# Optimization experiments

Hardware: AMD Instinct MI355X
Metric: run time of the kernel (lower is better)

The kernel has to match this reference:

```python
import jax, jax.numpy as jnp
import numpy as np

EPS = 1e-5

def _conv3x3(x, w, b):
    # NCHW, OIHW, 3x3 stride 1 pad 1
    y = jax.lax.conv_general_dilated(x, w, window_strides=(1, 1),
                                     padding=((1, 1), (1, 1)),
                                     dimension_numbers=('NCHW', 'OIHW', 'NCHW'))
    return y + b[None, :, None, None]

def _pool_upsample(x, k):
    # adaptive avg pool to (H/k, W/k) then nearest block-upsample back
    B, C, H, W = x.shape
    p = x.reshape(B, C, H // k, k, W // k, k).mean(axis=(3, 5))
    return jnp.repeat(jnp.repeat(p, k, axis=2), k, axis=3)

def setup_inputs() -> dict:
    key = jax.random.key(0)
    ks = jax.random.split(key, 12)
    B, C, H, W = 32, 8, 300, 300
    d = {
        'x': jax.random.normal(ks[0], (B, C, H, W), jnp.float32),
        'w5': jax.random.normal(ks[1], (8, 16, 3, 3), jnp.float32) * 0.1,
        'b5': jnp.zeros((8,), jnp.float32),
        'w10': jax.random.normal(ks[2], (8, 16, 3, 3), jnp.float32) * 0.1,
        'b10': jnp.zeros((8,), jnp.float32),
        'w15': jax.random.normal(ks[3], (8, 16, 3, 3), jnp.float32) * 0.1,
        'b15': jnp.zeros((8,), jnp.float32),
        'gw': jax.random.normal(ks[4], (8, 24, 3, 3), jnp.float32) * 0.1,
        'gb': jnp.zeros((8,), jnp.float32),
        'mw': jax.random.normal(ks[5], (8, 24, 3, 3), jnp.float32) * 0.1,
        'mb': jnp.zeros((8,), jnp.float32),
        'gamma': jnp.ones((8,), jnp.float32),
        'beta': jnp.zeros((8,), jnp.float32),
    }
    return d

def reference(x, w5, b5, w10, b10, w15, b15, gw, gb, mw, mb, gamma, beta):
    up5 = _pool_upsample(x, 5)    # [B,8,300,300]
    up10 = _pool_upsample(x, 10)
    up15 = _pool_upsample(x, 15)
    c5 = _conv3x3(jnp.concatenate([x, up5], axis=1), w5, b5)
    c10 = _conv3x3(jnp.concatenate([x, up10], axis=1), w10, b10)
    c15 = _conv3x3(jnp.concatenate([x, up15], axis=1), w15, b15)
    g_in = jnp.concatenate([c5, c10, c15], axis=1)  # [B,24,H,W]
    # gated conv, activation=None: conv(g_in) * sigmoid(mask_conv(g_in))
    y = _conv3x3(g_in, gw, gb) * jax.nn.sigmoid(_conv3x3(g_in, mw, mb))
    # batch norm (training-mode batch stats, biased var, as torch default)
    mean = y.mean(axis=(0, 2, 3), keepdims=True)
    var = ((y - mean) ** 2).mean(axis=(0, 2, 3), keepdims=True)
    y = (y - mean) * jax.lax.rsqrt(var + EPS)
    return y * gamma[None, :, None, None] + beta[None, :, None, None]
```

## Files before the change

kernel.cpp:

```cpp
#include <hip/hip_runtime.h>
#include <math.h>

typedef __bf16 bfrag __attribute__((ext_vector_type(8)));
typedef __bf16 bf16x4 __attribute__((ext_vector_type(4)));
typedef __bf16 bf16x8 __attribute__((ext_vector_type(8)));
typedef float f32x4 __attribute__((ext_vector_type(4)));

#define BN 32
#define HH 300
#define WW 300
#define HW 90000
#define NPX (BN * HW)

#define GX 10
#define GY 19

#define P5I_BYTE_OFF   0
#define P10I_BYTE_OFF  1843200
#define P15I_BYTE_OFF  2304000
#define CWB_BYTE_OFF   2508800
#define GWB_BYTE_OFF   2524160
#define STAT_BYTE_OFF  2531328
#define SS_BYTE_OFF    2539520
#define XBF_BYTE_OFF   2539584
#define XBF_END        (XBF_BYTE_OFF + (size_t)NPX * 16)

__device__ __forceinline__ short f2bf(float f) {
    union { float f; unsigned u; } v;
    v.f = f;
    unsigned r = v.u + 0x7FFF + ((v.u >> 16) & 1);
    return (short)(r >> 16);
}

__device__ __forceinline__ float bf2f(unsigned short s) {
    union { unsigned u; float f; } v;
    v.u = ((unsigned)s) << 16;
    return v.f;
}

__global__ void k_setup(const float* __restrict__ w5, const float* __restrict__ w10,
                        const float* __restrict__ w15, const float* __restrict__ gw,
                        const float* __restrict__ mw, short* __restrict__ cBg,
                        short* __restrict__ gBg, double* __restrict__ stats) {
    int t = threadIdx.x;
    for (int idx = t; idx < 7680; idx += 256) {
        int s = idx / 2560, rem = idx % 2560;
        int n = rem / 160, r2 = rem % 160;
        int tap = r2 / 16, ci = r2 % 16;
        float v = 0.f;
        if (n < 8 && tap < 9) {
            const float* W = (s == 0) ? w5 : ((s == 1) ? w10 : w15);
            v = W[(n * 16 + ci) * 9 + tap];
        }
        cBg[idx] = f2bf(v);
    }
    for (int idx = t; idx < 3584; idx += 256) {
        int n = idx / 224, r2 = idx % 224;
        int blk = r2 / 8, cj = r2 % 8;
        float v = 0.f;
        if (blk < 27) {
            int tap = blk / 3, ci24 = (blk % 3) * 8 + cj;
            if (n < 8) v = gw[(n * 24 + ci24) * 9 + tap];
            else       v = mw[((n - 8) * 24 + ci24) * 9 + tap];
        }
        gBg[idx] = f2bf(v);
    }
    for (int idx = t; idx < 16 * 64; idx += 256) stats[idx] = 0.0;
}

__global__ void k_pool5(const float* __restrict__ x, unsigned short* __restrict__ p5i) {
    int id = blockIdx.x * 256 + threadIdx.x;
    int bc = id / 3600, cell = id % 3600;
    int b = bc >> 3, c = bc & 7;
    int pi = cell / 60, pj = cell % 60;
    const float* rp = x + (size_t)bc * HW + pi * 5 * WW + pj * 5;
    float s = 0.f;
#pragma unroll
    for (int u = 0; u < 5; u++)
#pragma unroll
        for (int v = 0; v < 5; v++) s += rp[u * WW + v];
    p5i[((size_t)b * 3600 + cell) * 8 + c] = (unsigned short)f2bf(s * 0.04f);
}

__global__ __launch_bounds__(256) void k_prep(const float* __restrict__ x,
                                              unsigned short* __restrict__ xbf,
                                              unsigned short* __restrict__ p5i) {
    __shared__ float tf[8][5][304];
    const int t = threadIdx.x;
    const int pi = blockIdx.x, b = blockIdx.y;
    for (int idx = t; idx < 3000; idx += 256) {
        int ch = idx / 375, rem = idx % 375;
        int r = rem / 75, j = rem % 75;
        float4 v = *(const float4*)&x[((size_t)(b * 8 + ch) * HH + pi * 5 + r) * WW + 4 * j];
        *(float4*)&tf[ch][r][4 * j] = v;
    }
    __syncthreads();
    for (int idx = t; idx < 1500; idx += 256) {
        int r = idx / 300, c = idx - r * 300;
        bf16x8 pk;
#pragma unroll
        for (int ch = 0; ch < 8; ch++) pk[ch] = (__bf16)tf[ch][r][c];
        *(bf16x8*)&xbf[((size_t)b * HW + (pi * 5 + r) * WW + c) * 8] = pk;
    }
    for (int idx = t; idx < 512; idx += 256) {
        int ch = idx >> 6, pj = idx & 63;
        if (pj < 60) {
            float s = 0.f;
#pragma unroll
            for (int u = 0; u < 5; u++)
#pragma unroll
                for (int v = 0; v < 5; v++) s += tf[ch][u][pj * 5 + v];
            p5i[((size_t)b * 3600 + pi * 60 + pj) * 8 + ch] = (unsigned short)f2bf(s * 0.04f);
        }
    }
}

__global__ void k_poolD(const unsigned short* __restrict__ p5i,
                        unsigned short* __restrict__ p10i,
                        unsigned short* __restrict__ p15i) {
    int id = blockIdx.x * 256 + threadIdx.x;
    if (id < 230400) {
        int bc = id / 900, cell = id % 900;
        int b = bc >> 3, c = bc & 7;
        int pi = cell / 30, pj = cell % 30;
        const unsigned short* base = p5i + ((size_t)b * 3600) * 8 + c;
        float s = bf2f(base[((2 * pi) * 60 + 2 * pj) * 8]) +
                  bf2f(base[((2 * pi) * 60 + 2 * pj + 1) * 8]) +
                  bf2f(base[((2 * pi + 1) * 60 + 2 * pj) * 8]) +
                  bf2f(base[((2 * pi + 1) * 60 + 2 * pj + 1) * 8]);
        p10i[((size_t)b * 900 + cell) * 8 + c] = (unsigned short)f2bf(s * 0.25f);
    } else if (id < 332800) {
        int id2 = id - 230400;
        int bc = id2 / 400, cell = id2 % 400;
        int b = bc >> 3, c = bc & 7;
        int pi = cell / 20, pj = cell % 20;
        const unsigned short* base = p5i + ((size_t)b * 3600) * 8 + c;
        float s = 0.f;
#pragma unroll
        for (int u = 0; u < 3; u++)
#pragma unroll
            for (int v = 0; v < 3; v++)
                s += bf2f(base[((3 * pi + u) * 60 + 3 * pj + v) * 8]);
        p15i[((size_t)b * 400 + cell) * 8 + c] = (unsigned short)f2bf(s * (1.f / 9.f));
    }
}

template <int K, int PW>
__device__ __forceinline__ void up_load(const unsigned short* __restrict__ pooled,
                                        int b, int r0, int c0, int t, uint4* v) {
#pragma unroll
    for (int it = 0; it < 3; it++) {
        int idx = t + 256 * it;
        uint4 val = {0u, 0u, 0u, 0u};
        if (idx < 720) {
            int i = idx / 36, j = idx - i * 36;
            int ra = r0 - 2 + i, ca = c0 - 2 + j;
            if (ra >= 0 && ra < HH && ca >= 0 && ca < WW) {
                int pi = (int)((unsigned)ra / K);
                int pj = (int)((unsigned)ca / K);
                val = *(const uint4*)&pooled[((size_t)b * (PW * PW) + pi * PW + pj) * 8];
            }
        }
        v[it] = val;
    }
}

__device__ __forceinline__ void up_store(short* xuU, int t, const uint4* v) {
#pragma unroll
    for (int it = 0; it < 3; it++) {
        int idx = t + 256 * it;
        if (idx < 720) *(uint4*)&xuU[idx * 8] = v[it];
    }
}

__device__ __forceinline__ void c_phase(const short* xuX, const short* xuU,
                                        short* cwS,
                                        const unsigned short* __restrict__ cBs,
                                        const float* __restrict__ bias, int s,
                                        int r0, int c0, int lane, int wid, bool edge) {
    const int n = lane & 15, quad = lane >> 4;
    const int qh = quad >> 1, ql = quad & 1;
    const short* xbase = ql ? xuU : xuX;
    bfrag wfr[5];
    int dpoff[5];
#pragma unroll
    for (int km = 0; km < 5; km++) {
        int tapw = km * 2 + qh;
        int tapa = (tapw > 8) ? 8 : tapw;
        wfr[km] = *(const bfrag*)&cBs[(n * 10 + tapw) * 16 + ql * 8];
        dpoff[km] = ((tapa / 3) * 36 + tapa % 3) * 8;
    }
    float bO[4];
#pragma unroll
    for (int r = 0; r < 4; r++) bO[r] = bias[(quad & 1) * 4 + r];

    for (int g = wid; g < 39; g += 4) {
        int px = g * 16 + n;
        if (px > 611) px = 611;
        int rp = (int)((unsigned)px / 34u);
        int cp = px - rp * 34;
        int pb = (rp * 36 + cp) * 8;
        f32x4 acc = {0.f, 0.f, 0.f, 0.f};
#pragma unroll
        for (int km = 0; km < 5; km++)
            acc = __builtin_amdgcn_mfma_f32_16x16x32_bf16(
                wfr[km], *(const bfrag*)&xbase[pb + dpoff[km]], acc, 0, 0, 0);
        if (quad < 2) {
            bf16x4 pk;
#pragma unroll
            for (int r = 0; r < 4; r++) pk[r] = (__bf16)(acc[r] + bO[r]);
            if (edge) {
                int ra = r0 - 1 + rp, ca = c0 - 1 + cp;
                if (ra < 0 || ra >= HH || ca < 0 || ca >= WW) {
#pragma unroll
                    for (int r = 0; r < 4; r++) pk[r] = (__bf16)0.f;
                }
            }
            *(bf16x4*)&cwS[px * 24 + s * 8 + quad * 4] = pk;
        }
    }
}

template <bool XBF>
__global__ __launch_bounds__(256, 3) void k_fused(
    const float* __restrict__ x, const unsigned short* __restrict__ xbf,
    const unsigned short* __restrict__ p5i, const unsigned short* __restrict__ p10i,
    const unsigned short* __restrict__ p15i,
    const unsigned short* __restrict__ cBg, const unsigned short* __restrict__ gBg,
    const float* __restrict__ b5, const float* __restrict__ b10, const float* __restrict__ b15,
    const float* __restrict__ gb, const float* __restrict__ mb,
    float* __restrict__ out, double* __restrict__ stats) {
    __shared__ __align__(16) short xuX[720 * 8];
    __shared__ __align__(16) short xuU[720 * 8];
    __shared__ __align__(16) short cwS[612 * 24];

    const int b = blockIdx.z;
    const int r0 = blockIdx.y * 16, c0 = blockIdx.x * 32;
    const int t = threadIdx.x, lane = t & 63, wid = t >> 6;
    const bool edge = (blockIdx.x == 0) | (blockIdx.x == GX - 1) |
                      (blockIdx.y == 0) | (blockIdx.y == GY - 1);

    uint4 upv[3];
    up_load<5, 60>(p5i, b, r0, c0, t, upv);

    if constexpr (XBF) {
        for (int it = 0; it < 3; it++) {
            int idx = t + 256 * it;
            if (idx < 720) {
                int i = idx / 36, j = idx - i * 36;
                int ra = r0 - 2 + i, ca = c0 - 2 + j;
                uint4 v = {0u, 0u, 0u, 0u};
                if (ra >= 0 && ra < HH && ca >= 0 && ca < WW)
                    v = *(const uint4*)&xbf[((size_t)b * HW + ra * WW + ca) * 8];
                *(uint4*)&xuX[idx * 8] = v;
            }
        }
    } else {
        for (int idx = t; idx < 1440; idx += 256) {
            int cp = idx / 360, rem = idx % 360;
            int i = rem / 18, jp = rem % 18;
            int j = 2 * jp;
            int ra = r0 - 2 + i, ca = c0 - 2 + j;
            float2 v0 = {0.f, 0.f}, v1 = {0.f, 0.f};
            if (ra >= 0 && ra < HH && ca >= 0 && ca <= WW - 2) {
                size_t base = ((size_t)(b * 8 + 2 * cp) * HH + ra) * WW + ca;
                v0 = *(const float2*)&x[base];
                v1 = *(const float2*)&x[base + HW];
            }
            unsigned pA = (unsigned short)f2bf(v0.x) | ((unsigned)(unsigned short)f2bf(v1.x) << 16);
            unsigned pB = (unsigned short)f2bf(v0.y) | ((unsigned)(unsigned short)f2bf(v1.y) << 16);
            int px = i * 36 + j;
            *(unsigned*)&xuX[px * 8 + 2 * cp] = pA;
            *(unsigned*)&xuX[(px + 1) * 8 + 2 * cp] = pB;
        }
    }
    up_store(xuU, t, upv);
    __syncthreads();

    c_phase(xuX, xuU, cwS, cBg, b5, 0, r0, c0, lane, wid, edge);
    up_load<10, 30>(p10i, b, r0, c0, t, upv);
    __syncthreads();
    up_store(xuU, t, upv);
    __syncthreads();

    c_phase(xuX, xuU, cwS, cBg + 2560, b10, 1, r0, c0, lane, wid, edge);
    up_load<15, 20>(p15i, b, r0, c0, t, upv);
    __syncthreads();
    up_store(xuU, t, upv);
    __syncthreads();

    c_phase(xuX, xuU, cwS, cBg + 5120, b15, 2, r0, c0, lane, wid, edge);
    __syncthreads();

    const int n = lane & 15, quad = lane >> 4;
    bfrag gfr[7];
    int goff[7];
#pragma unroll
    for (int km = 0; km < 7; km++) {
        int blkw = km * 4 + quad;
        int blka = (blkw > 26) ? 26 : blkw;
        gfr[km] = *(const bfrag*)&gBg[(n * 28 + blkw) * 8];
        int tap = blka / 3, cig = blka - tap * 3;
        goff[km] = ((tap / 3) * 34 + tap % 3) * 24 + cig * 8;
    }
    float gO[4], mO[4];
#pragma unroll
    for (int r = 0; r < 4; r++) {
        gO[r] = gb[(quad & 1) * 4 + r];
        mO[r] = mb[(quad & 1) * 4 + r];
    }
    float ls[4] = {0.f, 0.f, 0.f, 0.f}, ls2[4] = {0.f, 0.f, 0.f, 0.f};

    for (int g = wid; g < 32; g += 4) {
        int px = g * 16 + n;
        int rr = px >> 5, cc = px & 31;
        int off0 = (rr * 34 + cc) * 24;
        f32x4 acc = {0.f, 0.f, 0.f, 0.f};
#pragma unroll
        for (int km = 0; km < 7; km++)
            acc = __builtin_amdgcn_mfma_f32_16x16x32_bf16(
                gfr[km], *(const bfrag*)&cwS[off0 + goff[km]], acc, 0, 0, 0);
        int ra = r0 + rr, ca = c0 + cc;
        bool wr = !edge || (ra < HH && ca < WW);
#pragma unroll
        for (int reg = 0; reg < 4; reg++) {
            float other = __shfl_xor(acc[reg], 32);
            if (quad < 2 && wr) {
                float G = acc[reg] + gO[reg];
                float M = other + mO[reg];
                float y = G * __builtin_amdgcn_rcpf(1.f + __expf(-M));
                int ch = quad * 4 + reg;
                out[(size_t)(b * 8 + ch) * HW + ra * WW + ca] = y;
                ls[reg] += y;
                ls2[reg] += y * y;
            }
        }
    }
#pragma unroll
    for (int m = 1; m < 16; m <<= 1) {
#pragma unroll
        for (int r = 0; r < 4; r++) {
            ls[r] += __shfl_xor(ls[r], m);
            ls2[r] += __shfl_xor(ls2[r], m);
        }
    }
    if (n == 0 && quad < 2) {
        int hash = (blockIdx.x + GX * blockIdx.y + GX * GY * blockIdx.z) & 63;
#pragma unroll
        for (int r = 0; r < 4; r++) {
            atomicAdd(&stats[(quad * 4 + r) * 64 + hash], (double)ls[r]);
            atomicAdd(&stats[(8 + quad * 4 + r) * 64 + hash], (double)ls2[r]);
        }
    }
}

__global__ void k_stats(const double* __restrict__ stats, const float* __restrict__ gamma,
                        const float* __restrict__ beta, float* __restrict__ ss) {
    __shared__ double tot[16];
    int t = threadIdx.x;
    if (t < 16) {
        double s = 0.0;
        for (int i = 0; i < 64; i++) s += stats[t * 64 + i];
        tot[t] = s;
    }
    __syncthreads();
    if (t < 8) {
        double N = (double)NPX;
        double mean = tot[t] / N;
        double var = tot[8 + t] / N - mean * mean;
        double scale = (double)gamma[t] / sqrt(var + 1e-5);
        ss[t] = (float)scale;
        ss[8 + t] = (float)((double)beta[t] - mean * scale);
    }
}

__global__ void k_norm(float* __restrict__ out, const float* __restrict__ ss) {
    int i = blockIdx.x * 256 + threadIdx.x;
    if (i < (BN * 8 * HW) / 4) {
        int plane = (i * 4) / HW;
        int ch = plane & 7;
        float sc = ss[ch], sh = ss[8 + ch];
        float4* p = (float4*)out + i;
        float4 v = *p;
        v.x = v.x * sc + sh;
        v.y = v.y * sc + sh;
        v.z = v.z * sc + sh;
        v.w = v.w * sc + sh;
        *p = v;
    }
}

extern "C" void kernel_launch(void* const* d_in, const int* in_sizes, int n_in,
                              void* d_out, int out_size, void* d_ws, size_t ws_size,
                              hipStream_t stream) {
    const float* x = (const float*)d_in[0];
    const float* w5 = (const float*)d_in[1];
    const float* b5 = (const float*)d_in[2];
    const float* w10 = (const float*)d_in[3];
    const float* b10 = (const float*)d_in[4];
    const float* w15 = (const float*)d_in[5];
    const float* b15 = (const float*)d_in[6];
    const float* gw = (const float*)d_in[7];
    const float* gb = (const float*)d_in[8];
    const float* mw = (const float*)d_in[9];
    const float* mb = (const float*)d_in[10];
    const float* gamma = (const float*)d_in[11];
    const float* beta = (const float*)d_in[12];

    float* out = (float*)d_out;
    unsigned short* p5i = (unsigned short*)((char*)d_ws + P5I_BYTE_OFF);
    unsigned short* p10i = (unsigned short*)((char*)d_ws + P10I_BYTE_OFF);
    unsigned short* p15i = (unsigned short*)((char*)d_ws + P15I_BYTE_OFF);
    short* cBg = (short*)((char*)d_ws + CWB_BYTE_OFF);
    short* gBg = (short*)((char*)d_ws + GWB_BYTE_OFF);
    double* stats = (double*)((char*)d_ws + STAT_BYTE_OFF);
    float* ss = (float*)((char*)d_ws + SS_BYTE_OFF);
    unsigned short* xbf = (unsigned short*)((char*)d_ws + XBF_BYTE_OFF);

    const bool use_xbf = (ws_size >= XBF_END);

    k_setup<<<1, 256, 0, stream>>>(w5, w10, w15, gw, mw, cBg, gBg, stats);
    if (use_xbf) {
        k_prep<<<dim3(60, 32), 256, 0, stream>>>(x, xbf, p5i);
    } else {
        k_pool5<<<3600, 256, 0, stream>>>(x, p5i);
    }
    k_poolD<<<1300, 256, 0, stream>>>(p5i, p10i, p15i);
    dim3 grid(GX, GY, BN);
    if (use_xbf) {
        k_fused<true><<<grid, 256, 0, stream>>>(x, xbf, p5i, p10i, p15i,
                                                (const unsigned short*)cBg, (const unsigned short*)gBg,
                                                b5, b10, b15, gb, mb, out, stats);
    } else {
        k_fused<false><<<grid, 256, 0, stream>>>(x, xbf, p5i, p10i, p15i,
                                                 (const unsigned short*)cBg, (const unsigned short*)gBg,
                                                 b5, b10, b15, gb, mb, out, stats);
    }
    k_stats<<<1, 64, 0, stream>>>(stats, gamma, beta, ss);
    k_norm<<<(BN * 8 * HW / 4 + 255) / 256, 256, 0, stream>>>(out, ss);
}
```

Measured before the change: 390.7 us.

## Shrink fused conv tile to 16x16 with planar per-branch LDS for higher occupancy

Changes the spatial tile from 16x32 to 16x16 (GX 10→19), which shrinks the LDS footprint of the input halo and the intermediate conv buffer, and raises the launch-bounds occupancy target from 3 to 5 blocks. The intermediate conv outputs move from an interleaved 24-channel layout to three separate 8-channel planes, with the gated-conv offsets recomputed to match. The sigmoid is now computed in the upper lanes before the cross-lane shuffle instead of after it, so that work is spread across both lane halves. In exchange, the smaller tile means more halo recomputation and redundant loads per output pixel.

After: 413.4 us. 1.06x slower.

```diff
diff --git a/kernel.cpp b/kernel.cpp
--- a/kernel.cpp
+++ b/kernel.cpp
@@ -12,8 +12,11 @@
 #define HW 90000
 #define NPX (BN * HW)
 
-#define GX 10
+#define GX 19
 #define GY 19
+#define CPX 324
+#define XPX 400
+#define CWSTRIDE 2592
 
 #define P5I_BYTE_OFF   0
 #define P10I_BYTE_OFF  1843200
@@ -149,11 +152,11 @@
 __device__ __forceinline__ void up_load(const unsigned short* __restrict__ pooled,
                                         int b, int r0, int c0, int t, uint4* v) {
 #pragma unroll
-    for (int it = 0; it < 3; it++) {
+    for (int it = 0; it < 2; it++) {
         int idx = t + 256 * it;
         uint4 val = {0u, 0u, 0u, 0u};
-        if (idx < 720) {
-            int i = idx / 36, j = idx - i * 36;
+        if (idx < XPX) {
+            int i = idx / 20, j = idx - i * 20;
             int ra = r0 - 2 + i, ca = c0 - 2 + j;
             if (ra >= 0 && ra < HH && ca >= 0 && ca < WW) {
                 int pi = (int)((unsigned)ra / K);
@@ -167,16 +170,16 @@
 
 __device__ __forceinline__ void up_store(short* xuU, int t, const uint4* v) {
 #pragma unroll
-    for (int it = 0; it < 3; it++) {
+    for (int it = 0; it < 2; it++) {
         int idx = t + 256 * it;
-        if (idx < 720) *(uint4*)&xuU[idx * 8] = v[it];
+        if (idx < XPX) *(uint4*)&xuU[idx * 8] = v[it];
     }
 }
 
 __device__ __forceinline__ void c_phase(const short* xuX, const short* xuU,
-                                        short* cwS,
+                                        short* cwP,
                                         const unsigned short* __restrict__ cBs,
-                                        const float* __restrict__ bias, int s,
+                                        const float* __restrict__ bias,
                                         int r0, int c0, int lane, int wid, bool edge) {
     const int n = lane & 15, quad = lane >> 4;
     const int qh = quad >> 1, ql = quad & 1;
@@ -188,18 +191,18 @@
         int tapw = km * 2 + qh;
         int tapa = (tapw > 8) ? 8 : tapw;
         wfr[km] = *(const bfrag*)&cBs[(n * 10 + tapw) * 16 + ql * 8];
-        dpoff[km] = ((tapa / 3) * 36 + tapa % 3) * 8;
+        dpoff[km] = ((tapa / 3) * 20 + tapa % 3) * 8;
     }
     float bO[4];
 #pragma unroll
     for (int r = 0; r < 4; r++) bO[r] = bias[(quad & 1) * 4 + r];
 
-    for (int g = wid; g < 39; g += 4) {
+    for (int g = wid; g < 21; g += 4) {
         int px = g * 16 + n;
-        if (px > 611) px = 611;
-        int rp = (int)((unsigned)px / 34u);
-        int cp = px - rp * 34;
-        int pb = (rp * 36 + cp) * 8;
+        if (px > 323) px = 323;
+        int rp = (int)((unsigned)px / 18u);
+        int cp = px - rp * 18;
+        int pb = (rp * 20 + cp) * 8;
         f32x4 acc = {0.f, 0.f, 0.f, 0.f};
 #pragma unroll
         for (int km = 0; km < 5; km++)
@@ -216,13 +219,13 @@
                     for (int r = 0; r < 4; r++) pk[r] = (__bf16)0.f;
                 }
             }
-            *(bf16x4*)&cwS[px * 24 + s * 8 + quad * 4] = pk;
+            *(bf16x4*)&cwP[px * 8 + quad * 4] = pk;
         }
     }
 }
 
 template <bool XBF>
-__global__ __launch_bounds__(256, 3) void k_fused(
+__global__ __launch_bounds__(256, 5) void k_fused(
     const float* __restrict__ x, const unsigned short* __restrict__ xbf,
     const unsigned short* __restrict__ p5i, const unsigned short* __restrict__ p10i,
     const unsigned short* __restrict__ p15i,
@@ -230,24 +233,25 @@
     const float* __restrict__ b5, const float* __restrict__ b10, const float* __restrict__ b15,
     const float* __restrict__ gb, const float* __restrict__ mb,
     float* __restrict__ out, double* __restrict__ stats) {
-    __shared__ __align__(16) short xuX[720 * 8];
-    __shared__ __align__(16) short xuU[720 * 8];
-    __shared__ __align__(16) short cwS[612 * 24];
+    __shared__ __align__(16) short xuX[XPX * 8];
+    __shared__ __align__(16) short xuU[XPX * 8];
+    __shared__ __align__(16) short cwS[3 * CWSTRIDE];
 
     const int b = blockIdx.z;
-    const int r0 = blockIdx.y * 16, c0 = blockIdx.x * 32;
+    const int r0 = blockIdx.y * 16, c0 = blockIdx.x * 16;
     const int t = threadIdx.x, lane = t & 63, wid = t >> 6;
     const bool edge = (blockIdx.x == 0) | (blockIdx.x == GX - 1) |
                       (blockIdx.y == 0) | (blockIdx.y == GY - 1);
 
-    uint4 upv[3];
+    uint4 upv[2];
     up_load<5, 60>(p5i, b, r0, c0, t, upv);
 
     if constexpr (XBF) {
-        for (int it = 0; it < 3; it++) {
+#pragma unroll
+        for (int it = 0; it < 2; it++) {
             int idx = t + 256 * it;
-            if (idx < 720) {
-                int i = idx / 36, j = idx - i * 36;
+            if (idx < XPX) {
+                int i = idx / 20, j = idx - i * 20;
                 int ra = r0 - 2 + i, ca = c0 - 2 + j;
                 uint4 v = {0u, 0u, 0u, 0u};
                 if (ra >= 0 && ra < HH && ca >= 0 && ca < WW)
@@ -256,9 +260,9 @@
             }
         }
     } else {
-        for (int idx = t; idx < 1440; idx += 256) {
-            int cp = idx / 360, rem = idx % 360;
-            int i = rem / 18, jp = rem % 18;
+        for (int idx = t; idx < 800; idx += 256) {
+            int cp = idx / 200, rem = idx % 200;
+            int i = rem / 10, jp = rem % 10;
             int j = 2 * jp;
             int ra = r0 - 2 + i, ca = c0 - 2 + j;
             float2 v0 = {0.f, 0.f}, v1 = {0.f, 0.f};
@@ -269,7 +273,7 @@
             }
             unsigned pA = (unsigned short)f2bf(v0.x) | ((unsigned)(unsigned short)f2bf(v1.x) << 16);
             unsigned pB = (unsigned short)f2bf(v0.y) | ((unsigned)(unsigned short)f2bf(v1.y) << 16);
-            int px = i * 36 + j;
+            int px = i * 20 + j;
             *(unsigned*)&xuX[px * 8 + 2 * cp] = pA;
             *(unsigned*)&xuX[(px + 1) * 8 + 2 * cp] = pB;
         }
@@ -277,19 +281,19 @@
     up_store(xuU, t, upv);
     __syncthreads();
 
-    c_phase(xuX, xuU, cwS, cBg, b5, 0, r0, c0, lane, wid, edge);
+    c_phase(xuX, xuU, cwS, cBg, b5, r0, c0, lane, wid, edge);
     up_load<10, 30>(p10i, b, r0, c0, t, upv);
     __syncthreads();
     up_store(xuU, t, upv);
     __syncthreads();
 
-    c_phase(xuX, xuU, cwS, cBg + 2560, b10, 1, r0, c0, lane, wid, edge);
+    c_phase(xuX, xuU, cwS + CWSTRIDE, cBg + 2560, b10, r0, c0, lane, wid, edge);
     up_load<15, 20>(p15i, b, r0, c0, t, upv);
     __syncthreads();
     up_store(xuU, t, upv);
     __syncthreads();
 
-    c_phase(xuX, xuU, cwS, cBg + 5120, b15, 2, r0, c0, lane, wid, edge);
+    c_phase(xuX, xuU, cwS + 2 * CWSTRIDE, cBg + 5120, b15, r0, c0, lane, wid, edge);
     __syncthreads();
 
     const int n = lane & 15, quad = lane >> 4;
@@ -301,7 +305,7 @@
         int blka = (blkw > 26) ? 26 : blkw;
         gfr[km] = *(const bfrag*)&gBg[(n * 28 + blkw) * 8];
         int tap = blka / 3, cig = blka - tap * 3;
-        goff[km] = ((tap / 3) * 34 + tap % 3) * 24 + cig * 8;
+        goff[km] = cig * CWSTRIDE + ((tap / 3) * 18 + tap % 3) * 8;
     }
     float gO[4], mO[4];
 #pragma unroll
@@ -311,24 +315,23 @@
     }
     float ls[4] = {0.f, 0.f, 0.f, 0.f}, ls2[4] = {0.f, 0.f, 0.f, 0.f};
 
-    for (int g = wid; g < 32; g += 4) {
-        int px = g * 16 + n;
-        int rr = px >> 5, cc = px & 31;
-        int off0 = (rr * 34 + cc) * 24;
+    for (int g = wid; g < 16; g += 4) {
+        int off0 = (g * 18 + n) * 8;
         f32x4 acc = {0.f, 0.f, 0.f, 0.f};
 #pragma unroll
         for (int km = 0; km < 7; km++)
             acc = __builtin_amdgcn_mfma_f32_16x16x32_bf16(
                 gfr[km], *(const bfrag*)&cwS[off0 + goff[km]], acc, 0, 0, 0);
-        int ra = r0 + rr, ca = c0 + cc;
+        int ra = r0 + g, ca = c0 + n;
         bool wr = !edge || (ra < HH && ca < WW);
 #pragma unroll
         for (int reg = 0; reg < 4; reg++) {
-            float other = __shfl_xor(acc[reg], 32);
+            float val;
+            if (quad < 2) val = acc[reg] + gO[reg];
+            else          val = __builtin_amdgcn_rcpf(1.f + __expf(-(acc[reg] + mO[reg])));
+            float other = __shfl_xor(val, 32);
             if (quad < 2 && wr) {
-                float G = acc[reg] + gO[reg];
-                float M = other + mO[reg];
-                float y = G * __builtin_amdgcn_rcpf(1.f + __expf(-M));
+                float y = val * other;
                 int ch = quad * 4 + reg;
                 out[(size_t)(b * 8 + ch) * HW + ra * WW + ca] = y;
                 ls[reg] += y;
```
